# Kernel optimization log

Hardware: AMD Instinct MI355X
Metric: run time of the kernel (lower is better)

The kernel has to match this reference:

```python
import jax, jax.numpy as jnp
import numpy as np

HW, B, C, NH, NC, HF, WF = 2500, 2, 256, 8, 6, 64, 176
DFF = 4 * C
EPS = 1e-5

def _layernorm(x, g, b):
    m = x.mean(-1, keepdims=True)
    v = ((x - m) ** 2).mean(-1, keepdims=True)
    return (x - m) / jnp.sqrt(v + EPS) * g + b

def _mha(q, kv, in_w, in_b, ow, ob):
    # q: [L,B,C], kv: [S,B,C] (batch_first=False, torch nn.MultiheadAttention)
    L, Bq, Cq = q.shape
    S = kv.shape[0]
    Dh = Cq // NH
    qp = (q @ in_w[:Cq].T + in_b[:Cq]).reshape(L, Bq, NH, Dh)
    kp = (kv @ in_w[Cq:2 * Cq].T + in_b[Cq:2 * Cq]).reshape(S, Bq, NH, Dh)
    vp = (kv @ in_w[2 * Cq:].T + in_b[2 * Cq:]).reshape(S, Bq, NH, Dh)
    att = jnp.einsum('lbhd,sbhd->bhls', qp, kp) * (1.0 / np.sqrt(Dh))
    att = jax.nn.softmax(att, axis=-1)
    out = jnp.einsum('bhls,sbhd->lbhd', att, vp).reshape(L, Bq, Cq)
    return out @ ow.T + ob

def _grid_sample_zeros(feat, grid):
    # feat: [B,N,C,H,W], grid: [B,N,Q,2] in [-1,1]; bilinear, align_corners=False, zero padding
    Bb, N, Cc, Hf, Wf = feat.shape
    Q = grid.shape[2]
    x = (grid[..., 0] + 1.0) * (Wf / 2.0) - 0.5
    y = (grid[..., 1] + 1.0) * (Hf / 2.0) - 0.5
    x0 = jnp.floor(x); y0 = jnp.floor(y)
    wx = x - x0; wy = y - y0
    x0i = x0.astype(jnp.int32); y0i = y0.astype(jnp.int32)
    ff = feat.reshape(Bb, N, Cc, Hf * Wf)
    def corner(xi, yi, w):
        valid = (xi >= 0) & (xi < Wf) & (yi >= 0) & (yi < Hf)
        idx = jnp.clip(yi, 0, Hf - 1) * Wf + jnp.clip(xi, 0, Wf - 1)  # [B,N,Q]
        g = jnp.take_along_axis(ff, jnp.broadcast_to(idx[:, :, None, :], (Bb, N, Cc, Q)), axis=-1)
        return g * (w * valid)[:, :, None, :]
    return (corner(x0i, y0i, (1.0 - wx) * (1.0 - wy)) + corner(x0i + 1, y0i, wx * (1.0 - wy))
            + corner(x0i, y0i + 1, (1.0 - wx) * wy) + corner(x0i + 1, y0i + 1, wx * wy))

def _forward(bev_queries, prev_bev, image_feat, reference_points, camera_intrinsics, camera_extrinsics,
             in_proj_w, in_proj_b, out_proj_w, out_proj_b, tsa_norm_g, tsa_norm_b,
             sca_w, sca_b, sca_norm_g, sca_norm_b, ffn_w1, ffn_b1, ffn_w2, ffn_b2, ffn_norm_g, ffn_norm_b):
    # TSA (dropout is identity in eval)
    tsa_out = _mha(bev_queries, prev_bev, in_proj_w, in_proj_b, out_proj_w, out_proj_b)
    x = _layernorm(bev_queries + tsa_out, tsa_norm_g, tsa_norm_b)
    # SCA: ego->camera->image projection
    R = camera_extrinsics[:, :, :3, :3]            # [B,N,3,3]
    t = camera_extrinsics[:, :, :3, 3]             # [B,N,3]
    R_e2c = jnp.swapaxes(R, -1, -2)
    t_e2c = -jnp.einsum('bnij,bnj->bni', R_e2c, t)
    pts_cam = jnp.einsum('bnij,qj->bnqi', R_e2c, reference_points) + t_e2c[:, :, None, :]  # [B,N,Q,3]
    pts_img = jnp.einsum('bnij,bnqj->bnqi', camera_intrinsics, pts_cam)
    uv = pts_img[..., :2] / jnp.maximum(pts_img[..., 2:3], 1e-5)
    grid = jnp.stack([2.0 * uv[..., 0] / WF - 1.0, 2.0 * uv[..., 1] / HF - 1.0], axis=-1)  # [B,N,Q,2]
    Bq = bev_queries.shape[1]
    feat_r = image_feat.reshape(Bq, NC, C, HF, WF)
    sampled = _grid_sample_zeros(feat_r, grid).mean(axis=1)   # [B,C,Q]
    sampled = jnp.transpose(sampled, (2, 0, 1))               # [Q,B,C]
    sca_out = sampled @ sca_w.T + sca_b
    x = _layernorm(x + sca_out, sca_norm_g, sca_norm_b)
    # FFN (torch nn.GELU default = exact erf)
    h = jax.nn.gelu(x @ ffn_w1 + ffn_b1, approximate=False)
    ffn_out = h @ ffn_w2 + ffn_b2
    return _layernorm(x + ffn_out, ffn_norm_g, ffn_norm_b)

def setup_inputs():
    key = jax.random.key(0)
    ks = jax.random.split(key, 16)
    f = jnp.float32
    s = 0.02
    return {
        'bev_queries': jax.random.normal(ks[0], (HW, B, C), f),
        'prev_bev': jax.random.normal(ks[1], (HW, B, C), f),
        'image_feat': jax.random.normal(ks[2], (B * NC, C, HF, WF), f),
        'reference_points': jax.random.normal(ks[3], (HW, 3), f) * 20.0,
        'camera_intrinsics': jax.random.normal(ks[4], (B, NC, 3, 3), f),
        'camera_extrinsics': jax.random.normal(ks[5], (B, NC, 4, 4), f),
        'spatial_shapes': jnp.array([[HF, WF]], jnp.int32),
        'in_proj_w': jax.random.normal(ks[6], (3 * C, C), f) * s,
        'in_proj_b': jnp.zeros((3 * C,), f),
        'out_proj_w': jax.random.normal(ks[7], (C, C), f) * s,
        'out_proj_b': jnp.zeros((C,), f),
        'tsa_norm_g': jnp.ones((C,), f), 'tsa_norm_b': jnp.zeros((C,), f),
        'sca_w': jax.random.normal(ks[8], (C, C), f) * s,
        'sca_b': jnp.zeros((C,), f),
        'sca_norm_g': jnp.ones((C,), f), 'sca_norm_b': jnp.zeros((C,), f),
        'ffn_w1': jax.random.normal(ks[9], (C, DFF), f) * s,
        'ffn_b1': jnp.zeros((DFF,), f),
        'ffn_w2': jax.random.normal(ks[10], (DFF, C), f) * s,
        'ffn_b2': jnp.zeros((C,), f),
        'ffn_norm_g': jnp.ones((C,), f), 'ffn_norm_b': jnp.zeros((C,), f),
    }

def reference(bev_queries, prev_bev, image_feat, reference_points, camera_intrinsics, camera_extrinsics,
              in_proj_w, in_proj_b, out_proj_w, out_proj_b, tsa_norm_g, tsa_norm_b,
              sca_w, sca_b, sca_norm_g, sca_norm_b, ffn_w1, ffn_b1, ffn_w2, ffn_b2, ffn_norm_g, ffn_norm_b,
              spatial_shapes):
    return _forward(bev_queries, prev_bev, image_feat, reference_points, camera_intrinsics, camera_extrinsics,
                    in_proj_w, in_proj_b, out_proj_w, out_proj_b, tsa_norm_g, tsa_norm_b,
                    sca_w, sca_b, sca_norm_g, sca_norm_b, ffn_w1, ffn_b1, ffn_w2, ffn_b2, ffn_norm_g, ffn_norm_b)
```

## Files before the change

kernel.cpp:

```cpp
#include <hip/hip_runtime.h>

typedef unsigned short u16;
typedef __attribute__((ext_vector_type(8))) __bf16 bf8_t;
typedef __attribute__((ext_vector_type(4))) float f4_t;

union bf8u { u16 u[8]; bf8_t v; uint4 q; };

__device__ __forceinline__ float bf2f(u16 v) {
  return __uint_as_float(((unsigned int)v) << 16);
}
__device__ __forceinline__ u16 f2bf(float f) {
  union { __bf16 h; u16 u; } c;
  c.h = (__bf16)f;
  return c.u;
}
__device__ __forceinline__ float bflo(unsigned int w) { return __uint_as_float(w << 16); }
__device__ __forceinline__ float bfhi(unsigned int w) { return __uint_as_float(w & 0xFFFF0000u); }
__device__ __forceinline__ float ldf1(const void* p, size_t i, int isf32) {
  return isf32 ? ((const float*)p)[i] : bf2f(((const u16*)p)[i]);
}

#define LQ    2500
#define LQP   2560
#define BB    2
#define CC    256
#define NCC   6
#define HFF   64
#define WFF   176
#define DFF   1024
#define MROWS 5000

#define WB_UV   256
#define WB_WQKV 240256
#define WB_WOP  633472
#define WB_WSC  764544
#define WB_WF1  895616
#define WB_WF2  1419904
#define WB_S1   1944192
#define WB_S2   (WB_S1 + 2621440)
#define WB_S3   (WB_S2 + 2621440)
#define WB_VT   (WB_S3 + 2621440)
#define WB_H    WB_S2
#define WB_Y3   (WB_S2 + 10485760)

__global__ void detect_k(const u16* __restrict__ rp, int* __restrict__ flag) {
  int bad = 0;
  for (int i = threadIdx.x; i < 7500; i += 64) {
    float v = bf2f(rp[i]);
    if (!(fabsf(v) < 1e6f)) bad = 1;
  }
  int anybad = __any(bad);
  if (threadIdx.x == 0) flag[0] = anybad ? 1 : 0;
}

struct WDesc {
  const void* src[6];
  u16* dst[6];
  int n[6];
  int mode[6];
  int Kd[6], Nd[6];
};
__global__ __launch_bounds__(256) void cvtw_k(WDesc d, const int* __restrict__ flag) {
  const int df = flag[0];
  const int i = blockIdx.y;
  const int n = d.n[i];
  for (int j = blockIdx.x * 256 + threadIdx.x; j < n; j += gridDim.x * 256) {
    if (d.mode[i] == 2) {
      const int row = j / (LQP - LQ), col = LQ + j % (LQP - LQ);
      d.dst[i][(size_t)row * LQP + col] = 0;
    } else if (d.mode[i] == 1) {
      const int K = d.Kd[i], N = d.Nd[i];
      const int nn = j / K, kk = j - nn * K;
      d.dst[i][j] = f2bf(ldf1(d.src[i], (size_t)kk * N + nn, df));
    } else {
      d.dst[i][j] = f2bf(ldf1(d.src[i], j, df));
    }
  }
}

template<int KTPL, int XRAW, int ACT, int RES, int STORE_T>
__global__ __launch_bounds__(64) void gemm_nl(
    const void* __restrict__ Xv, const u16* __restrict__ W,
    const void* __restrict__ bias, size_t boff,
    const void* __restrict__ resv,
    u16* __restrict__ Y, int M, int N, const int* __restrict__ flag)
{
  const int df = flag[0];
  const int lane = threadIdx.x;
  const int ln15 = lane & 15, l4 = lane >> 4;
  const int m0 = blockIdx.x * 16, n0 = blockIdx.y * 64;
  const int am = min(m0 + ln15, M - 1);

  f4_t acc[4];
#pragma unroll
  for (int nt = 0; nt < 4; ++nt) acc[nt] = (f4_t){0.f, 0.f, 0.f, 0.f};

#pragma unroll 8
  for (int k0 = 0; k0 < KTPL; k0 += 32) {
    bf8u a;
    if (XRAW && df) {
      const float* p = (const float*)Xv + (size_t)am * KTPL + k0 + l4 * 8;
      float4 r0 = *(const float4*)p, r1 = *(const float4*)(p + 4);
      a.u[0]=f2bf(r0.x); a.u[1]=f2bf(r0.y); a.u[2]=f2bf(r0.z); a.u[3]=f2bf(r0.w);
      a.u[4]=f2bf(r1.x); a.u[5]=f2bf(r1.y); a.u[6]=f2bf(r1.z); a.u[7]=f2bf(r1.w);
    } else {
      a.q = *(const uint4*)((const u16*)Xv + (size_t)am * KTPL + k0 + l4 * 8);
    }
#pragma unroll
    for (int nt = 0; nt < 4; ++nt) {
      bf8u b;
      b.q = *(const uint4*)&W[(size_t)(n0 + nt * 16 + ln15) * KTPL + k0 + l4 * 8];
      acc[nt] = __builtin_amdgcn_mfma_f32_16x16x32_bf16(a.v, b.v, acc[nt], 0, 0, 0);
    }
  }
#pragma unroll
  for (int nt = 0; nt < 4; ++nt) {
    const int gn = n0 + nt * 16 + ln15;
    const float bv = ldf1(bias, boff + gn, df);
#pragma unroll
    for (int r = 0; r < 4; ++r) {
      const int gm = m0 + l4 * 4 + r;
      if (gm < M) {
        float x = acc[nt][r] + bv;
        if (ACT) x = 0.5f * x * (1.f + erff(x * 0.70710678118654752f));
        if (RES == 1)      x += bf2f(((const u16*)resv)[(size_t)gm * N + gn]);
        else if (RES == 2) x += ldf1(resv, (size_t)gm * N + gn, df);
        if (STORE_T) {
          const int tt = gm >> 1;
          const int tx = tt & 63;
          const int tp = (tx & 35) | ((tx & 12) << 1) | ((tx & 16) >> 2);
          Y[(size_t)(gn + (gm & 1) * 256) * LQP + ((tt & ~63) | tp)] = f2bf(x);
        } else {
          Y[(size_t)gm * N + gn] = f2bf(x);
        }
      }
    }
  }
}

#define TPW 10
__global__ __launch_bounds__(256) void attn_mf(
    const u16* __restrict__ Qw, const u16* __restrict__ Kw,
    const u16* __restrict__ Vt, u16* __restrict__ Ow)
{
  __shared__ float sO[4][16][33];
  __shared__ float sM[4][16];
  __shared__ float sL[4][16];
  const int t = threadIdx.x;
  const int lane = t & 63, w = t >> 6;
  const int ln15 = lane & 15, l4 = lane >> 4;
  const int q0 = blockIdx.x * 16;
  const int by = blockIdx.y;
  const int b = by >> 3, h = by & 7;
  const float SCL2E = 0.25505654481f;

  bf8u aq;
  {
    const int qrow = min(q0 + ln15, LQ - 1);
    bf8u qr; qr.q = *(const uint4*)&Qw[((size_t)qrow * BB + b) * CC + h * 32 + l4 * 8];
#pragma unroll
    for (int i = 0; i < 8; ++i) aq.u[i] = f2bf(bf2f(qr.u[i]) * SCL2E);
  }

  f4_t oacc[2];
  oacc[0] = (f4_t){0.f,0.f,0.f,0.f};
  oacc[1] = (f4_t){0.f,0.f,0.f,0.f};
  float m_r = -1e30f;
  float l_r = 0.f;

  for (int kt = w * TPW; kt < w * TPW + TPW; ++kt) {
    const int kb = kt * 64;
    bf8u av[2][2];
#pragma unroll
    for (int m = 0; m < 2; ++m)
#pragma unroll
      for (int dt = 0; dt < 2; ++dt)
        av[m][dt].q = *(const uint4*)&Vt[(size_t)(by * 32 + dt * 16 + ln15) * LQP + kb + m * 32 + l4 * 8];
    f4_t sv[4];
#pragma unroll
    for (int nt = 0; nt < 4; ++nt) {
      bf8u bk;
      bk.q = *(const uint4*)&Kw[((size_t)(kb + nt * 16 + ln15) * BB + b) * CC + h * 32 + l4 * 8];
      f4_t z = (f4_t){0.f,0.f,0.f,0.f};
      sv[nt] = __builtin_amdgcn_mfma_f32_16x16x32_bf16(bk.v, aq.v, z, 0, 0, 0);
    }
    float p[4][4];
    if (kb + 64 <= LQ) {
#pragma unroll
      for (int nt = 0; nt < 4; ++nt)
#pragma unroll
        for (int r = 0; r < 4; ++r) p[nt][r] = sv[nt][r];
    } else {
#pragma unroll
      for (int nt = 0; nt < 4; ++nt)
#pragma unroll
        for (int r = 0; r < 4; ++r)
          p[nt][r] = (kb + nt * 16 + l4 * 4 + r < LQ) ? sv[nt][r] : -1e30f;
    }
    const float m0 = fmaxf(fmaxf(p[0][0], p[0][1]), fmaxf(p[0][2], p[0][3]));
    const float m1 = fmaxf(fmaxf(p[1][0], p[1][1]), fmaxf(p[1][2], p[1][3]));
    const float m2 = fmaxf(fmaxf(p[2][0], p[2][1]), fmaxf(p[2][2], p[2][3]));
    const float m3 = fmaxf(fmaxf(p[3][0], p[3][1]), fmaxf(p[3][2], p[3][3]));
    float mloc = fmaxf(fmaxf(m0, m1), fmaxf(m2, m3));
    mloc = fmaxf(mloc, __shfl_xor(mloc, 16));
    mloc = fmaxf(mloc, __shfl_xor(mloc, 32));
    const float mn = fmaxf(m_r, mloc);
    const float alpha = __builtin_amdgcn_exp2f(m_r - mn);
    m_r = mn;
    float s = 0.f;
#pragma unroll
    for (int nt = 0; nt < 4; ++nt) {
#pragma unroll
      for (int r = 0; r < 4; ++r) {
        const float e = __builtin_amdgcn_exp2f(p[nt][r] - mn);
        p[nt][r] = e; s += e;
      }
    }
    l_r = l_r * alpha + s;
#pragma unroll
    for (int r = 0; r < 4; ++r) { oacc[0][r] *= alpha; oacc[1][r] *= alpha; }
#pragma unroll
    for (int m = 0; m < 2; ++m) {
      bf8u pb;
#pragma unroll
      for (int i = 0; i < 8; ++i) pb.u[i] = f2bf(p[2 * m + (i >> 2)][i & 3]);
#pragma unroll
      for (int dt = 0; dt < 2; ++dt)
        oacc[dt] = __builtin_amdgcn_mfma_f32_16x16x32_bf16(av[m][dt].v, pb.v, oacc[dt], 0, 0, 0);
    }
  }
  l_r += __shfl_xor(l_r, 16);
  l_r += __shfl_xor(l_r, 32);
#pragma unroll
  for (int dt = 0; dt < 2; ++dt)
#pragma unroll
    for (int r = 0; r < 4; ++r)
      sO[w][ln15][dt * 16 + l4 * 4 + r] = oacc[dt][r];
  if (l4 == 0) { sM[w][ln15] = m_r; sL[w][ln15] = l_r; }
  __syncthreads();
#pragma unroll
  for (int i = t; i < 512; i += 256) {
    const int row = i >> 5, col = i & 31;
    const float M = fmaxf(fmaxf(sM[0][row], sM[1][row]), fmaxf(sM[2][row], sM[3][row]));
    float l = 0.f, O = 0.f;
#pragma unroll
    for (int w4 = 0; w4 < 4; ++w4) {
      const float sc = __builtin_amdgcn_exp2f(sM[w4][row] - M);
      l += sc * sL[w4][row];
      O += sc * sO[w4][row][col];
    }
    const int q = q0 + row;
    if (q < LQ)
      Ow[((size_t)q * BB + b) * CC + h * 32 + col] = f2bf(O / l);
  }
}

template<int TOOUT>
__global__ __launch_bounds__(256) void ln_k(const u16* __restrict__ X,
    const void* __restrict__ g, const void* __restrict__ be,
    void* __restrict__ Yv, int rows, const int* __restrict__ flag)
{
  const int df = flag[0];
  const int lane = threadIdx.x & 63;
  const int row = blockIdx.x * 4 + (threadIdx.x >> 6);
  if (row >= rows) return;
  uint2 raw = *(const uint2*)(X + (size_t)row * CC + lane * 4);
  float vx = bflo(raw.x), vy = bfhi(raw.x), vz = bflo(raw.y), vw = bfhi(raw.y);
  float s = vx + vy + vz + vw;
#pragma unroll
  for (int o = 1; o < 64; o <<= 1) s += __shfl_xor(s, o);
  const float mean = s * 0.00390625f;
  const float dx = vx - mean, dy = vy - mean, dz = vz - mean, dw = vw - mean;
  float sq = dx*dx + dy*dy + dz*dz + dw*dw;
#pragma unroll
  for (int o = 1; o < 64; o <<= 1) sq += __shfl_xor(sq, o);
  const float rstd = rsqrtf(sq * 0.00390625f + 1e-5f);
  const float g0 = ldf1(g, lane*4+0, df), g1 = ldf1(g, lane*4+1, df);
  const float g2 = ldf1(g, lane*4+2, df), g3 = ldf1(g, lane*4+3, df);
  const float b0 = ldf1(be, lane*4+0, df), b1 = ldf1(be, lane*4+1, df);
  const float b2 = ldf1(be, lane*4+2, df), b3 = ldf1(be, lane*4+3, df);
  const float y0 = dx * rstd * g0 + b0;
  const float y1 = dy * rstd * g1 + b1;
  const float y2 = dz * rstd * g2 + b2;
  const float y3 = dw * rstd * g3 + b3;
  if (TOOUT && df) {
    float* yp = (float*)Yv + (size_t)row * CC + lane * 4;
    *(float4*)yp = make_float4(y0, y1, y2, y3);
  } else {
    u16* yp = (u16*)Yv + (size_t)row * CC + lane * 4;
    unsigned int lo = (unsigned int)f2bf(y0) | ((unsigned int)f2bf(y1) << 16);
    unsigned int hi = (unsigned int)f2bf(y2) | ((unsigned int)f2bf(y3) << 16);
    *(uint2*)yp = make_uint2(lo, hi);
  }
}

__global__ __launch_bounds__(256) void uv_k(
    const void* __restrict__ refp, const void* __restrict__ intr,
    const void* __restrict__ extr, float* __restrict__ uv,
    const int* __restrict__ flag)
{
  const int df = flag[0];
  const int idx = blockIdx.x * 256 + threadIdx.x;
  if (idx >= BB * NCC * LQ) return;
  const int bc = idx / LQ;
  const int q = idx - bc * LQ;
  float R[3][3], tv[3], Kc[3][3], p[3];
#pragma unroll
  for (int i = 0; i < 3; ++i) {
#pragma unroll
    for (int j = 0; j < 3; ++j) {
      R[i][j] = ldf1(extr, bc*16 + i*4 + j, df);
      Kc[i][j] = ldf1(intr, bc*9 + i*3 + j, df);
    }
    tv[i] = ldf1(extr, bc*16 + i*4 + 3, df);
  }
#pragma unroll
  for (int j = 0; j < 3; ++j) p[j] = ldf1(refp, q*3 + j, df) - tv[j];
  float pc[3];
#pragma unroll
  for (int i = 0; i < 3; ++i) pc[i] = R[0][i]*p[0] + R[1][i]*p[1] + R[2][i]*p[2];
  float im[3];
#pragma unroll
  for (int i = 0; i < 3; ++i) im[i] = Kc[i][0]*pc[0] + Kc[i][1]*pc[1] + Kc[i][2]*pc[2];
  const float z = fmaxf(im[2], 1e-5f);
  uv[(size_t)idx*2 + 0] = im[0] / z - 0.5f;
  uv[(size_t)idx*2 + 1] = im[1] / z - 0.5f;
}

__global__ __launch_bounds__(256) void samp_k(
    const void* __restrict__ feat, const float* __restrict__ uv,
    u16* __restrict__ S, const int* __restrict__ flag)
{
  const int df = flag[0];
  const int c = blockIdx.x;
  const int b = blockIdx.y / 5;
  const int ch = blockIdx.y % 5;
  const int qend = min((ch + 1) * 500, LQ);
  for (int q = ch * 500 + threadIdx.x; q < qend; q += 256) {
    float acc = 0.f;
#pragma unroll
    for (int cam = 0; cam < NCC; ++cam) {
      const int bc = b * NCC + cam;
      const float x = uv[((size_t)bc * LQ + q) * 2 + 0];
      const float y = uv[((size_t)bc * LQ + q) * 2 + 1];
      const float xf = floorf(x), yf = floorf(y);
      const int x0 = (int)xf, y0 = (int)yf;
      const float wx = x - xf, wy = y - yf;
      const size_t base = ((size_t)bc * CC + c) * (HFF * WFF);
      const bool vx0 = (x0 >= 0) & (x0 < WFF);
      const bool vx1 = (x0 + 1 >= 0) & (x0 + 1 < WFF);
      const bool vy0 = (y0 >= 0) & (y0 < HFF);
      const bool vy1 = (y0 + 1 >= 0) & (y0 + 1 < HFF);
      if (vy0) {
        const size_t rb = base + (size_t)y0 * WFF;
        if (vx0) acc += (1.f - wx) * (1.f - wy) * ldf1(feat, rb + x0, df);
        if (vx1) acc += wx * (1.f - wy) * ldf1(feat, rb + x0 + 1, df);
      }
      if (vy1) {
        const size_t rb = base + (size_t)(y0 + 1) * WFF;
        if (vx0) acc += (1.f - wx) * wy * ldf1(feat, rb + x0, df);
        if (vx1) acc += wx * wy * ldf1(feat, rb + x0 + 1, df);
      }
    }
    S[((size_t)q * BB + b) * CC + c] = f2bf(acc * (1.f / 6.f));
  }
}

extern "C" void kernel_launch(void* const* d_in, const int* in_sizes, int n_in,
                              void* d_out, int out_size, void* d_ws, size_t ws_size,
                              hipStream_t stream) {
  (void)in_sizes; (void)n_in; (void)out_size; (void)ws_size;
  char* base = (char*)d_ws;
  int* flag = (int*)base;
  float* UV = (float*)(base + WB_UV);
  u16* WQKV = (u16*)(base + WB_WQKV);
  u16* WOP  = (u16*)(base + WB_WOP);
  u16* WSC  = (u16*)(base + WB_WSC);
  u16* WF1  = (u16*)(base + WB_WF1);
  u16* WF2  = (u16*)(base + WB_WF2);
  u16* S1 = (u16*)(base + WB_S1);
  u16* S2 = (u16*)(base + WB_S2);
  u16* S3 = (u16*)(base + WB_S3);
  u16* VT = (u16*)(base + WB_VT);
  u16* H  = (u16*)(base + WB_H);
  u16* Y3 = (u16*)(base + WB_Y3);

  detect_k<<<1, 64, 0, stream>>>((const u16*)d_in[3], flag);

  WDesc wd;
  wd.src[0] = d_in[7];  wd.dst[0] = WQKV; wd.n[0] = 196608; wd.mode[0] = 0; wd.Kd[0] = 0;    wd.Nd[0] = 0;
  wd.src[1] = d_in[9];  wd.dst[1] = WOP;  wd.n[1] = 65536;  wd.mode[1] = 0; wd.Kd[1] = 0;    wd.Nd[1] = 0;
  wd.src[2] = d_in[13]; wd.dst[2] = WSC;  wd.n[2] = 65536;  wd.mode[2] = 0; wd.Kd[2] = 0;    wd.Nd[2] = 0;
  wd.src[3] = d_in[17]; wd.dst[3] = WF1;  wd.n[3] = 262144; wd.mode[3] = 1; wd.Kd[3] = 256;  wd.Nd[3] = 1024;
  wd.src[4] = d_in[19]; wd.dst[4] = WF2;  wd.n[4] = 262144; wd.mode[4] = 1; wd.Kd[4] = 1024; wd.Nd[4] = 256;
  wd.src[5] = nullptr;  wd.dst[5] = VT;   wd.n[5] = 512 * (LQP - LQ); wd.mode[5] = 2; wd.Kd[5] = 0; wd.Nd[5] = 0;
  cvtw_k<<<dim3(128, 6), 256, 0, stream>>>(wd, flag);

  uv_k<<<(BB * NCC * LQ + 255) / 256, 256, 0, stream>>>(d_in[3], d_in[4], d_in[5], UV, flag);

  gemm_nl<256,1,0,0,0><<<dim3(313, 4), 64, 0, stream>>>(d_in[0], WQKV,          d_in[8], 0,   nullptr, S1, MROWS, CC, flag);
  gemm_nl<256,1,0,0,0><<<dim3(313, 4), 64, 0, stream>>>(d_in[1], WQKV + 65536,  d_in[8], 256, nullptr, S2, MROWS, CC, flag);
  gemm_nl<256,1,0,0,1><<<dim3(313, 4), 64, 0, stream>>>(d_in[1], WQKV + 131072, d_in[8], 512, nullptr, VT, MROWS, CC, flag);

  attn_mf<<<dim3(157, 16), 256, 0, stream>>>(S1, S2, VT, S3);

  gemm_nl<256,0,0,2,0><<<dim3(313, 4), 64, 0, stream>>>(S3, WOP, d_in[10], 0, d_in[0], S1, MROWS, CC, flag);
  ln_k<0><<<1250, 256, 0, stream>>>(S1, d_in[11], d_in[12], S2, MROWS, flag);

  samp_k<<<dim3(CC, BB * 5), 256, 0, stream>>>(d_in[2], UV, VT, flag);

  gemm_nl<256,0,0,1,0><<<dim3(313, 4), 64, 0, stream>>>(VT, WSC, d_in[14], 0, S2, S3, MROWS, CC, flag);
  ln_k<0><<<1250, 256, 0, stream>>>(S3, d_in[15], d_in[16], S1, MROWS, flag);

  gemm_nl<256,0,1,0,0><<<dim3(313, 16), 64, 0, stream>>>(S1, WF1, d_in[18], 0, nullptr, H,  MROWS, DFF, flag);
  gemm_nl<1024,0,0,1,0><<<dim3(313, 4),  64, 0, stream>>>(H,  WF2, d_in[20], 0, S1,      Y3, MROWS, CC,  flag);
  ln_k<1><<<1250, 256, 0, stream>>>(Y3, d_in[21], d_in[22], d_out, MROWS, flag);
}
```

Before: 515.8 us.

## Fuse QKV projections, prefetch K in attention, lazy softmax rescale, narrower GEMM tiles

Merges the three Q/K/V projection GEMMs into one launch. The attention kernel now prefetches the next K tile into registers, raises wave priority around the MFMA blocks, and only rescales the running output when the max grows by more than 8 (in log2 units). The N-tile width of gemm_nl becomes a template parameter, and the 256-wide-output GEMMs use 16-column tiles so more blocks are launched. Together these aim to cut launch overhead, hide memory latency in attention and raise occupancy on the small GEMMs. The tradeoffs are more redundant A-row loads per GEMM block and a lazy softmax that leaves exponents up to 2^8 before renormalising.

Result: no change. 519.7 us (+0.8%).

```diff
diff --git a/kernel.cpp b/kernel.cpp
--- a/kernel.cpp
+++ b/kernel.cpp
@@ -78,7 +78,7 @@
   }
 }
 
-template<int KTPL, int XRAW, int ACT, int RES, int STORE_T>
+template<int KTPL, int XRAW, int ACT, int RES, int STORE_T, int NT>
 __global__ __launch_bounds__(64) void gemm_nl(
     const void* __restrict__ Xv, const u16* __restrict__ W,
     const void* __restrict__ bias, size_t boff,
@@ -88,12 +88,12 @@
   const int df = flag[0];
   const int lane = threadIdx.x;
   const int ln15 = lane & 15, l4 = lane >> 4;
-  const int m0 = blockIdx.x * 16, n0 = blockIdx.y * 64;
+  const int m0 = blockIdx.x * 16, n0 = blockIdx.y * (NT * 16);
   const int am = min(m0 + ln15, M - 1);
 
-  f4_t acc[4];
-#pragma unroll
-  for (int nt = 0; nt < 4; ++nt) acc[nt] = (f4_t){0.f, 0.f, 0.f, 0.f};
+  f4_t acc[NT];
+#pragma unroll
+  for (int nt = 0; nt < NT; ++nt) acc[nt] = (f4_t){0.f, 0.f, 0.f, 0.f};
 
 #pragma unroll 8
   for (int k0 = 0; k0 < KTPL; k0 += 32) {
@@ -107,14 +107,14 @@
       a.q = *(const uint4*)((const u16*)Xv + (size_t)am * KTPL + k0 + l4 * 8);
     }
 #pragma unroll
-    for (int nt = 0; nt < 4; ++nt) {
+    for (int nt = 0; nt < NT; ++nt) {
       bf8u b;
       b.q = *(const uint4*)&W[(size_t)(n0 + nt * 16 + ln15) * KTPL + k0 + l4 * 8];
       acc[nt] = __builtin_amdgcn_mfma_f32_16x16x32_bf16(a.v, b.v, acc[nt], 0, 0, 0);
     }
   }
 #pragma unroll
-  for (int nt = 0; nt < 4; ++nt) {
+  for (int nt = 0; nt < NT; ++nt) {
     const int gn = n0 + nt * 16 + ln15;
     const float bv = ldf1(bias, boff + gn, df);
 #pragma unroll
@@ -138,6 +138,67 @@
   }
 }
 
+__global__ __launch_bounds__(64) void gemm_qkv(
+    const void* __restrict__ Xq, const void* __restrict__ Xkv,
+    const u16* __restrict__ Wqkv, const void* __restrict__ bias,
+    u16* __restrict__ Qo, u16* __restrict__ Ko, u16* __restrict__ Vt,
+    const int* __restrict__ flag)
+{
+  const int df = flag[0];
+  const int lane = threadIdx.x;
+  const int ln15 = lane & 15, l4 = lane >> 4;
+  const int which = blockIdx.y >> 2;
+  const int n0 = (blockIdx.y & 3) * 64;
+  const void* Xv = (which == 0) ? Xq : Xkv;
+  const u16* W = Wqkv + (size_t)which * 65536;
+  const int m0 = blockIdx.x * 16;
+  const int am = min(m0 + ln15, MROWS - 1);
+
+  f4_t acc[4];
+#pragma unroll
+  for (int nt = 0; nt < 4; ++nt) acc[nt] = (f4_t){0.f, 0.f, 0.f, 0.f};
+
+#pragma unroll 8
+  for (int k0 = 0; k0 < CC; k0 += 32) {
+    bf8u a;
+    if (df) {
+      const float* p = (const float*)Xv + (size_t)am * CC + k0 + l4 * 8;
+      float4 r0 = *(const float4*)p, r1 = *(const float4*)(p + 4);
+      a.u[0]=f2bf(r0.x); a.u[1]=f2bf(r0.y); a.u[2]=f2bf(r0.z); a.u[3]=f2bf(r0.w);
+      a.u[4]=f2bf(r1.x); a.u[5]=f2bf(r1.y); a.u[6]=f2bf(r1.z); a.u[7]=f2bf(r1.w);
+    } else {
+      a.q = *(const uint4*)((const u16*)Xv + (size_t)am * CC + k0 + l4 * 8);
+    }
+#pragma unroll
+    for (int nt = 0; nt < 4; ++nt) {
+      bf8u b;
+      b.q = *(const uint4*)&W[(size_t)(n0 + nt * 16 + ln15) * CC + k0 + l4 * 8];
+      acc[nt] = __builtin_amdgcn_mfma_f32_16x16x32_bf16(a.v, b.v, acc[nt], 0, 0, 0);
+    }
+  }
+#pragma unroll
+  for (int nt = 0; nt < 4; ++nt) {
+    const int gn = n0 + nt * 16 + ln15;
+    const float bv = ldf1(bias, which * 256 + gn, df);
+#pragma unroll
+    for (int r = 0; r < 4; ++r) {
+      const int gm = m0 + l4 * 4 + r;
+      if (gm < MROWS) {
+        const float x = acc[nt][r] + bv;
+        if (which == 2) {
+          const int tt = gm >> 1;
+          const int tx = tt & 63;
+          const int tp = (tx & 35) | ((tx & 12) << 1) | ((tx & 16) >> 2);
+          Vt[(size_t)(gn + (gm & 1) * 256) * LQP + ((tt & ~63) | tp)] = f2bf(x);
+        } else {
+          u16* Y = (which == 0) ? Qo : Ko;
+          Y[(size_t)gm * CC + gn] = f2bf(x);
+        }
+      }
+    }
+  }
+}
+
 #define TPW 10
 __global__ __launch_bounds__(256) void attn_mf(
     const u16* __restrict__ Qw, const u16* __restrict__ Kw,
@@ -168,22 +229,39 @@
   float m_r = -1e30f;
   float l_r = 0.f;
 
-  for (int kt = w * TPW; kt < w * TPW + TPW; ++kt) {
+  const int kt0 = w * TPW;
+  const u16* Kbase = &Kw[(size_t)b * CC + h * 32 + l4 * 8];
+  const u16* Vbase = &Vt[(size_t)(by * 32 + ln15) * LQP + l4 * 8];
+
+  bf8u bkn[4];
+#pragma unroll
+  for (int nt = 0; nt < 4; ++nt)
+    bkn[nt].q = *(const uint4*)&Kbase[(size_t)(kt0 * 64 + nt * 16 + ln15) * CC];
+
+  for (int kt = kt0; kt < kt0 + TPW; ++kt) {
     const int kb = kt * 64;
     bf8u av[2][2];
 #pragma unroll
     for (int m = 0; m < 2; ++m)
 #pragma unroll
       for (int dt = 0; dt < 2; ++dt)
-        av[m][dt].q = *(const uint4*)&Vt[(size_t)(by * 32 + dt * 16 + ln15) * LQP + kb + m * 32 + l4 * 8];
+        av[m][dt].q = *(const uint4*)&Vbase[(size_t)(dt * 16) * LQP + kb + m * 32];
+    bf8u bk[4];
+#pragma unroll
+    for (int nt = 0; nt < 4; ++nt) bk[nt] = bkn[nt];
+    if (kt + 1 < kt0 + TPW) {
+#pragma unroll
+      for (int nt = 0; nt < 4; ++nt)
+        bkn[nt].q = *(const uint4*)&Kbase[(size_t)(kb + 64 + nt * 16 + ln15) * CC];
+    }
     f4_t sv[4];
+    __builtin_amdgcn_s_setprio(1);
 #pragma unroll
     for (int nt = 0; nt < 4; ++nt) {
-      bf8u bk;
-      bk.q = *(const uint4*)&Kw[((size_t)(kb + nt * 16 + ln15) * BB + b) * CC + h * 32 + l4 * 8];
       f4_t z = (f4_t){0.f,0.f,0.f,0.f};
-      sv[nt] = __builtin_amdgcn_mfma_f32_16x16x32_bf16(bk.v, aq.v, z, 0, 0, 0);
-    }
+      sv[nt] = __builtin_amdgcn_mfma_f32_16x16x32_bf16(bk[nt].v, aq.v, z, 0, 0, 0);
+    }
+    __builtin_amdgcn_s_setprio(0);
     float p[4][4];
     if (kb + 64 <= LQ) {
 #pragma unroll
@@ -204,21 +282,25 @@
     float mloc = fmaxf(fmaxf(m0, m1), fmaxf(m2, m3));
     mloc = fmaxf(mloc, __shfl_xor(mloc, 16));
     mloc = fmaxf(mloc, __shfl_xor(mloc, 32));
-    const float mn = fmaxf(m_r, mloc);
-    const float alpha = __builtin_amdgcn_exp2f(m_r - mn);
-    m_r = mn;
+    if (__any(mloc > m_r + 8.f)) {
+      const float mn = fmaxf(m_r, mloc);
+      const float alpha = __builtin_amdgcn_exp2f(m_r - mn);
+      m_r = mn;
+      l_r *= alpha;
+#pragma unroll
+      for (int r = 0; r < 4; ++r) { oacc[0][r] *= alpha; oacc[1][r] *= alpha; }
+    }
     float s = 0.f;
 #pragma unroll
     for (int nt = 0; nt < 4; ++nt) {
 #pragma unroll
       for (int r = 0; r < 4; ++r) {
-        const float e = __builtin_amdgcn_exp2f(p[nt][r] - mn);
+        const float e = __builtin_amdgcn_exp2f(p[nt][r] - m_r);
         p[nt][r] = e; s += e;
       }
     }
-    l_r = l_r * alpha + s;
-#pragma unroll
-    for (int r = 0; r < 4; ++r) { oacc[0][r] *= alpha; oacc[1][r] *= alpha; }
+    l_r += s;
+    __builtin_amdgcn_s_setprio(1);
 #pragma unroll
     for (int m = 0; m < 2; ++m) {
       bf8u pb;
@@ -228,6 +310,7 @@
       for (int dt = 0; dt < 2; ++dt)
         oacc[dt] = __builtin_amdgcn_mfma_f32_16x16x32_bf16(av[m][dt].v, pb.v, oacc[dt], 0, 0, 0);
     }
+    __builtin_amdgcn_s_setprio(0);
   }
   l_r += __shfl_xor(l_r, 16);
   l_r += __shfl_xor(l_r, 32);
@@ -398,21 +481,19 @@
 
   uv_k<<<(BB * NCC * LQ + 255) / 256, 256, 0, stream>>>(d_in[3], d_in[4], d_in[5], UV, flag);
 
-  gemm_nl<256,1,0,0,0><<<dim3(313, 4), 64, 0, stream>>>(d_in[0], WQKV,          d_in[8], 0,   nullptr, S1, MROWS, CC, flag);
-  gemm_nl<256,1,0,0,0><<<dim3(313, 4), 64, 0, stream>>>(d_in[1], WQKV + 65536,  d_in[8], 256, nullptr, S2, MROWS, CC, flag);
-  gemm_nl<256,1,0,0,1><<<dim3(313, 4), 64, 0, stream>>>(d_in[1], WQKV + 131072, d_in[8], 512, nullptr, VT, MROWS, CC, flag);
+  gemm_qkv<<<dim3(313, 12), 64, 0, stream>>>(d_in[0], d_in[1], WQKV, d_in[8], S1, S2, VT, flag);
 
   attn_mf<<<dim3(157, 16), 256, 0, stream>>>(S1, S2, VT, S3);
 
-  gemm_nl<256,0,0,2,0><<<dim3(313, 4), 64, 0, stream>>>(S3, WOP, d_in[10], 0, d_in[0], S1, MROWS, CC, flag);
+  gemm_nl<256,0,0,2,0,1><<<dim3(313, 16), 64, 0, stream>>>(S3, WOP, d_in[10], 0, d_in[0], S1, MROWS, CC, flag);
   ln_k<0><<<1250, 256, 0, stream>>>(S1, d_in[11], d_in[12], S2, MROWS, flag);
 
   samp_k<<<dim3(CC, BB * 5), 256, 0, stream>>>(d_in[2], UV, VT, flag);
 
-  gemm_nl<256,0,0,1,0><<<dim3(313, 4), 64, 0, stream>>>(VT, WSC, d_in[14], 0, S2, S3, MROWS, CC, flag);
+  gemm_nl<256,0,0,1,0,1><<<dim3(313, 16), 64, 0, stream>>>(VT, WSC, d_in[14], 0, S2, S3, MROWS, CC, flag);
   ln_k<0><<<1250, 256, 0, stream>>>(S3, d_in[15], d_in[16], S1, MROWS, flag);
 
-  gemm_nl<256,0,1,0,0><<<dim3(313, 16), 64, 0, stream>>>(S1, WF1, d_in[18], 0, nullptr, H,  MROWS, DFF, flag);
-  gemm_nl<1024,0,0,1,0><<<dim3(313, 4),  64, 0, stream>>>(H,  WF2, d_in[20], 0, S1,      Y3, MROWS, CC,  flag);
+  gemm_nl<256,0,1,0,0,4><<<dim3(313, 16), 64, 0, stream>>>(S1, WF1, d_in[18], 0, nullptr, H,  MROWS, DFF, flag);
+  gemm_nl<1024,0,0,1,0,1><<<dim3(313, 16), 64, 0, stream>>>(H,  WF2, d_in[20], 0, S1,      Y3, MROWS, CC,  flag);
   ln_k<1><<<1250, 256, 0, stream>>>(Y3, d_in[21], d_in[22], d_out, MROWS, flag);
 }
```

## Use LDS-tiled 128x128 GEMM, fuse QKV projections, prefetch K and lazy-rescale in attention

Applied to the files above, without the earlier changes.

Replaces the one-wave 16x64 GEMM with a 256-thread 128x128 tile GEMM that stages A/B through shared memory with register prefetch. The three QKV projections become one launch over a 768-wide output, with inputs pre-converted to bf16 in the weight conversion kernel. The attention kernel now prefetches the next K tile, raises wave priority around MFMAs, and only rescales the running accumulator when the max grows by more than a threshold. Larger tiles cut global reloads, but the N=256 GEMMs launch only 80 blocks, which may underfill the GPU.

Measured after the change: 550.9 us. 1.07x slower.

```diff
diff --git a/kernel.cpp b/kernel.cpp
--- a/kernel.cpp
+++ b/kernel.cpp
@@ -42,6 +42,8 @@
 #define WB_VT   (WB_S3 + 2621440)
 #define WB_H    WB_S2
 #define WB_Y3   (WB_S2 + 10485760)
+#define WB_XQ   WB_Y3
+#define WB_XKV  (WB_Y3 + 2621440)
 
 __global__ void detect_k(const u16* __restrict__ rp, int* __restrict__ flag) {
   int bad = 0;
@@ -54,18 +56,27 @@
 }
 
 struct WDesc {
-  const void* src[6];
-  u16* dst[6];
-  int n[6];
-  int mode[6];
-  int Kd[6], Nd[6];
+  const void* src[8];
+  u16* dst[8];
+  int n[8];
+  int mode[8];
+  int Kd[8], Nd[8];
 };
 __global__ __launch_bounds__(256) void cvtw_k(WDesc d, const int* __restrict__ flag) {
   const int df = flag[0];
   const int i = blockIdx.y;
   const int n = d.n[i];
   for (int j = blockIdx.x * 256 + threadIdx.x; j < n; j += gridDim.x * 256) {
-    if (d.mode[i] == 2) {
+    if (d.mode[i] == 3) {
+      if (df) {
+        const float4 r = ((const float4*)d.src[i])[j];
+        const unsigned int lo = (unsigned int)f2bf(r.x) | ((unsigned int)f2bf(r.y) << 16);
+        const unsigned int hi = (unsigned int)f2bf(r.z) | ((unsigned int)f2bf(r.w) << 16);
+        ((uint2*)d.dst[i])[j] = make_uint2(lo, hi);
+      } else {
+        ((uint2*)d.dst[i])[j] = ((const uint2*)d.src[i])[j];
+      }
+    } else if (d.mode[i] == 2) {
       const int row = j / (LQP - LQ), col = LQ + j % (LQP - LQ);
       d.dst[i][(size_t)row * LQP + col] = 0;
     } else if (d.mode[i] == 1) {
@@ -78,60 +89,102 @@
   }
 }
 
-template<int KTPL, int XRAW, int ACT, int RES, int STORE_T>
-__global__ __launch_bounds__(64) void gemm_nl(
-    const void* __restrict__ Xv, const u16* __restrict__ W,
-    const void* __restrict__ bias, size_t boff,
+#define LDP 40
+template<int KT, int ACT, int RES, int QKV>
+__global__ __launch_bounds__(256) void gemm_t(
+    const u16* __restrict__ Xa, const u16* __restrict__ Xb,
+    const u16* __restrict__ W, const void* __restrict__ bias, size_t boff,
     const void* __restrict__ resv,
-    u16* __restrict__ Y, int M, int N, const int* __restrict__ flag)
+    u16* __restrict__ Y, u16* __restrict__ Yk, u16* __restrict__ Yv,
+    int M, int N, const int* __restrict__ flag)
 {
+  __shared__ __align__(16) u16 sA[128 * LDP];
+  __shared__ __align__(16) u16 sB[128 * LDP];
   const int df = flag[0];
-  const int lane = threadIdx.x;
+  const int t = threadIdx.x;
+  const int lane = t & 63, w = t >> 6;
   const int ln15 = lane & 15, l4 = lane >> 4;
-  const int m0 = blockIdx.x * 16, n0 = blockIdx.y * 64;
-  const int am = min(m0 + ln15, M - 1);
-
-  f4_t acc[4];
-#pragma unroll
-  for (int nt = 0; nt < 4; ++nt) acc[nt] = (f4_t){0.f, 0.f, 0.f, 0.f};
-
-#pragma unroll 8
-  for (int k0 = 0; k0 < KTPL; k0 += 32) {
-    bf8u a;
-    if (XRAW && df) {
-      const float* p = (const float*)Xv + (size_t)am * KTPL + k0 + l4 * 8;
-      float4 r0 = *(const float4*)p, r1 = *(const float4*)(p + 4);
-      a.u[0]=f2bf(r0.x); a.u[1]=f2bf(r0.y); a.u[2]=f2bf(r0.z); a.u[3]=f2bf(r0.w);
-      a.u[4]=f2bf(r1.x); a.u[5]=f2bf(r1.y); a.u[6]=f2bf(r1.z); a.u[7]=f2bf(r1.w);
-    } else {
-      a.q = *(const uint4*)((const u16*)Xv + (size_t)am * KTPL + k0 + l4 * 8);
-    }
-#pragma unroll
-    for (int nt = 0; nt < 4; ++nt) {
-      bf8u b;
-      b.q = *(const uint4*)&W[(size_t)(n0 + nt * 16 + ln15) * KTPL + k0 + l4 * 8];
-      acc[nt] = __builtin_amdgcn_mfma_f32_16x16x32_bf16(a.v, b.v, acc[nt], 0, 0, 0);
-    }
-  }
-#pragma unroll
-  for (int nt = 0; nt < 4; ++nt) {
-    const int gn = n0 + nt * 16 + ln15;
+  const int wm = w & 1, wn = w >> 1;
+  const int m0 = blockIdx.x * 128, n0 = blockIdx.y * 128;
+  const u16* X = (QKV && n0 >= 256) ? Xb : Xa;
+
+  const int r0 = t >> 2, seg = t & 3;
+  const int gr0 = min(m0 + r0, M - 1);
+  const int gr1 = min(m0 + r0 + 64, M - 1);
+  const u16* Asrc0 = X + (size_t)gr0 * KT + seg * 8;
+  const u16* Asrc1 = X + (size_t)gr1 * KT + seg * 8;
+  const u16* Bsrc0 = W + (size_t)(n0 + r0) * KT + seg * 8;
+  const u16* Bsrc1 = W + (size_t)(n0 + r0 + 64) * KT + seg * 8;
+  u16* Adst0 = &sA[r0 * LDP + seg * 8];
+  u16* Adst1 = &sA[(r0 + 64) * LDP + seg * 8];
+  u16* Bdst0 = &sB[r0 * LDP + seg * 8];
+  u16* Bdst1 = &sB[(r0 + 64) * LDP + seg * 8];
+
+  f4_t acc[4][4];
+#pragma unroll
+  for (int mi = 0; mi < 4; ++mi)
+#pragma unroll
+    for (int ni = 0; ni < 4; ++ni) acc[mi][ni] = (f4_t){0.f, 0.f, 0.f, 0.f};
+
+  uint4 ra0 = *(const uint4*)Asrc0;
+  uint4 ra1 = *(const uint4*)Asrc1;
+  uint4 rb0 = *(const uint4*)Bsrc0;
+  uint4 rb1 = *(const uint4*)Bsrc1;
+
+  for (int k0 = 0; k0 < KT; k0 += 32) {
+    __syncthreads();
+    *(uint4*)Adst0 = ra0;  *(uint4*)Adst1 = ra1;
+    *(uint4*)Bdst0 = rb0;  *(uint4*)Bdst1 = rb1;
+    __syncthreads();
+    bf8u a[4], b[4];
+#pragma unroll
+    for (int mi = 0; mi < 4; ++mi)
+      a[mi].q = *(const uint4*)&sA[(wm * 64 + mi * 16 + ln15) * LDP + l4 * 8];
+#pragma unroll
+    for (int ni = 0; ni < 4; ++ni)
+      b[ni].q = *(const uint4*)&sB[(wn * 64 + ni * 16 + ln15) * LDP + l4 * 8];
+    if (k0 + 32 < KT) {
+      ra0 = *(const uint4*)(Asrc0 + k0 + 32);
+      ra1 = *(const uint4*)(Asrc1 + k0 + 32);
+      rb0 = *(const uint4*)(Bsrc0 + k0 + 32);
+      rb1 = *(const uint4*)(Bsrc1 + k0 + 32);
+    }
+#pragma unroll
+    for (int mi = 0; mi < 4; ++mi)
+#pragma unroll
+      for (int ni = 0; ni < 4; ++ni)
+        acc[mi][ni] = __builtin_amdgcn_mfma_f32_16x16x32_bf16(a[mi].v, b[ni].v, acc[mi][ni], 0, 0, 0);
+  }
+
+#pragma unroll
+  for (int ni = 0; ni < 4; ++ni) {
+    const int gn = n0 + wn * 64 + ni * 16 + ln15;
     const float bv = ldf1(bias, boff + gn, df);
 #pragma unroll
-    for (int r = 0; r < 4; ++r) {
-      const int gm = m0 + l4 * 4 + r;
-      if (gm < M) {
-        float x = acc[nt][r] + bv;
-        if (ACT) x = 0.5f * x * (1.f + erff(x * 0.70710678118654752f));
-        if (RES == 1)      x += bf2f(((const u16*)resv)[(size_t)gm * N + gn]);
-        else if (RES == 2) x += ldf1(resv, (size_t)gm * N + gn, df);
-        if (STORE_T) {
-          const int tt = gm >> 1;
-          const int tx = tt & 63;
-          const int tp = (tx & 35) | ((tx & 12) << 1) | ((tx & 16) >> 2);
-          Y[(size_t)(gn + (gm & 1) * 256) * LQP + ((tt & ~63) | tp)] = f2bf(x);
-        } else {
-          Y[(size_t)gm * N + gn] = f2bf(x);
+    for (int mi = 0; mi < 4; ++mi) {
+#pragma unroll
+      for (int r = 0; r < 4; ++r) {
+        const int gm = m0 + wm * 64 + mi * 16 + l4 * 4 + r;
+        if (gm < M) {
+          float x = acc[mi][ni][r] + bv;
+          if (ACT) x = 0.5f * x * (1.f + erff(x * 0.70710678118654752f));
+          if (RES == 1)      x += bf2f(((const u16*)resv)[(size_t)gm * N + gn]);
+          else if (RES == 2) x += ldf1(resv, (size_t)gm * N + gn, df);
+          if (QKV) {
+            const int which = n0 >> 8;
+            const int cn = gn & 255;
+            if (which == 2) {
+              const int tt = gm >> 1, tx = tt & 63;
+              const int tp = (tx & 35) | ((tx & 12) << 1) | ((tx & 16) >> 2);
+              Yv[(size_t)(cn + (gm & 1) * 256) * LQP + ((tt & ~63) | tp)] = f2bf(x);
+            } else if (which == 1) {
+              Yk[(size_t)gm * 256 + cn] = f2bf(x);
+            } else {
+              Y[(size_t)gm * 256 + cn] = f2bf(x);
+            }
+          } else {
+            Y[(size_t)gm * N + gn] = f2bf(x);
+          }
         }
       }
     }
@@ -168,22 +221,39 @@
   float m_r = -1e30f;
   float l_r = 0.f;
 
-  for (int kt = w * TPW; kt < w * TPW + TPW; ++kt) {
+  const int kt0 = w * TPW;
+  const u16* Kbase = &Kw[(size_t)b * CC + h * 32 + l4 * 8];
+  const u16* Vbase = &Vt[(size_t)(by * 32 + ln15) * LQP + l4 * 8];
+
+  bf8u bkn[4];
+#pragma unroll
+  for (int nt = 0; nt < 4; ++nt)
+    bkn[nt].q = *(const uint4*)&Kbase[(size_t)(kt0 * 64 + nt * 16 + ln15) * CC];
+
+  for (int kt = kt0; kt < kt0 + TPW; ++kt) {
     const int kb = kt * 64;
     bf8u av[2][2];
 #pragma unroll
     for (int m = 0; m < 2; ++m)
 #pragma unroll
       for (int dt = 0; dt < 2; ++dt)
-        av[m][dt].q = *(const uint4*)&Vt[(size_t)(by * 32 + dt * 16 + ln15) * LQP + kb + m * 32 + l4 * 8];
+        av[m][dt].q = *(const uint4*)&Vbase[(size_t)(dt * 16) * LQP + kb + m * 32];
+    bf8u bk[4];
+#pragma unroll
+    for (int nt = 0; nt < 4; ++nt) bk[nt] = bkn[nt];
+    if (kt + 1 < kt0 + TPW) {
+#pragma unroll
+      for (int nt = 0; nt < 4; ++nt)
+        bkn[nt].q = *(const uint4*)&Kbase[(size_t)(kb + 64 + nt * 16 + ln15) * CC];
+    }
     f4_t sv[4];
+    __builtin_amdgcn_s_setprio(1);
 #pragma unroll
     for (int nt = 0; nt < 4; ++nt) {
-      bf8u bk;
-      bk.q = *(const uint4*)&Kw[((size_t)(kb + nt * 16 + ln15) * BB + b) * CC + h * 32 + l4 * 8];
       f4_t z = (f4_t){0.f,0.f,0.f,0.f};
-      sv[nt] = __builtin_amdgcn_mfma_f32_16x16x32_bf16(bk.v, aq.v, z, 0, 0, 0);
-    }
+      sv[nt] = __builtin_amdgcn_mfma_f32_16x16x32_bf16(bk[nt].v, aq.v, z, 0, 0, 0);
+    }
+    __builtin_amdgcn_s_setprio(0);
     float p[4][4];
     if (kb + 64 <= LQ) {
 #pragma unroll
@@ -204,21 +274,25 @@
     float mloc = fmaxf(fmaxf(m0, m1), fmaxf(m2, m3));
     mloc = fmaxf(mloc, __shfl_xor(mloc, 16));
     mloc = fmaxf(mloc, __shfl_xor(mloc, 32));
-    const float mn = fmaxf(m_r, mloc);
-    const float alpha = __builtin_amdgcn_exp2f(m_r - mn);
-    m_r = mn;
+    if (__any(mloc > m_r + 8.f)) {
+      const float mn = fmaxf(m_r, mloc);
+      const float alpha = __builtin_amdgcn_exp2f(m_r - mn);
+      m_r = mn;
+      l_r *= alpha;
+#pragma unroll
+      for (int r = 0; r < 4; ++r) { oacc[0][r] *= alpha; oacc[1][r] *= alpha; }
+    }
     float s = 0.f;
 #pragma unroll
     for (int nt = 0; nt < 4; ++nt) {
 #pragma unroll
       for (int r = 0; r < 4; ++r) {
-        const float e = __builtin_amdgcn_exp2f(p[nt][r] - mn);
+        const float e = __builtin_amdgcn_exp2f(p[nt][r] - m_r);
         p[nt][r] = e; s += e;
       }
     }
-    l_r = l_r * alpha + s;
-#pragma unroll
-    for (int r = 0; r < 4; ++r) { oacc[0][r] *= alpha; oacc[1][r] *= alpha; }
+    l_r += s;
+    __builtin_amdgcn_s_setprio(1);
 #pragma unroll
     for (int m = 0; m < 2; ++m) {
       bf8u pb;
@@ -228,6 +302,7 @@
       for (int dt = 0; dt < 2; ++dt)
         oacc[dt] = __builtin_amdgcn_mfma_f32_16x16x32_bf16(av[m][dt].v, pb.v, oacc[dt], 0, 0, 0);
     }
+    __builtin_amdgcn_s_setprio(0);
   }
   l_r += __shfl_xor(l_r, 16);
   l_r += __shfl_xor(l_r, 32);
@@ -384,35 +459,37 @@
   u16* VT = (u16*)(base + WB_VT);
   u16* H  = (u16*)(base + WB_H);
   u16* Y3 = (u16*)(base + WB_Y3);
+  u16* XQ  = (u16*)(base + WB_XQ);
+  u16* XKV = (u16*)(base + WB_XKV);
 
   detect_k<<<1, 64, 0, stream>>>((const u16*)d_in[3], flag);
 
   WDesc wd;
-  wd.src[0] = d_in[7];  wd.dst[0] = WQKV; wd.n[0] = 196608; wd.mode[0] = 0; wd.Kd[0] = 0;    wd.Nd[0] = 0;
-  wd.src[1] = d_in[9];  wd.dst[1] = WOP;  wd.n[1] = 65536;  wd.mode[1] = 0; wd.Kd[1] = 0;    wd.Nd[1] = 0;
-  wd.src[2] = d_in[13]; wd.dst[2] = WSC;  wd.n[2] = 65536;  wd.mode[2] = 0; wd.Kd[2] = 0;    wd.Nd[2] = 0;
+  wd.src[0] = d_in[7];  wd.dst[0] = WQKV; wd.n[0] = 49152;  wd.mode[0] = 3; wd.Kd[0] = 0;    wd.Nd[0] = 0;
+  wd.src[1] = d_in[9];  wd.dst[1] = WOP;  wd.n[1] = 16384;  wd.mode[1] = 3; wd.Kd[1] = 0;    wd.Nd[1] = 0;
+  wd.src[2] = d_in[13]; wd.dst[2] = WSC;  wd.n[2] = 16384;  wd.mode[2] = 3; wd.Kd[2] = 0;    wd.Nd[2] = 0;
   wd.src[3] = d_in[17]; wd.dst[3] = WF1;  wd.n[3] = 262144; wd.mode[3] = 1; wd.Kd[3] = 256;  wd.Nd[3] = 1024;
   wd.src[4] = d_in[19]; wd.dst[4] = WF2;  wd.n[4] = 262144; wd.mode[4] = 1; wd.Kd[4] = 1024; wd.Nd[4] = 256;
   wd.src[5] = nullptr;  wd.dst[5] = VT;   wd.n[5] = 512 * (LQP - LQ); wd.mode[5] = 2; wd.Kd[5] = 0; wd.Nd[5] = 0;
-  cvtw_k<<<dim3(128, 6), 256, 0, stream>>>(wd, flag);
+  wd.src[6] = d_in[0];  wd.dst[6] = XQ;   wd.n[6] = 320000; wd.mode[6] = 3; wd.Kd[6] = 0;    wd.Nd[6] = 0;
+  wd.src[7] = d_in[1];  wd.dst[7] = XKV;  wd.n[7] = 320000; wd.mode[7] = 3; wd.Kd[7] = 0;    wd.Nd[7] = 0;
+  cvtw_k<<<dim3(128, 8), 256, 0, stream>>>(wd, flag);
 
   uv_k<<<(BB * NCC * LQ + 255) / 256, 256, 0, stream>>>(d_in[3], d_in[4], d_in[5], UV, flag);
 
-  gemm_nl<256,1,0,0,0><<<dim3(313, 4), 64, 0, stream>>>(d_in[0], WQKV,          d_in[8], 0,   nullptr, S1, MROWS, CC, flag);
-  gemm_nl<256,1,0,0,0><<<dim3(313, 4), 64, 0, stream>>>(d_in[1], WQKV + 65536,  d_in[8], 256, nullptr, S2, MROWS, CC, flag);
-  gemm_nl<256,1,0,0,1><<<dim3(313, 4), 64, 0, stream>>>(d_in[1], WQKV + 131072, d_in[8], 512, nullptr, VT, MROWS, CC, flag);
+  gemm_t<256,0,0,1><<<dim3(40, 6), 256, 0, stream>>>(XQ, XKV, WQKV, d_in[8], 0, nullptr, S1, S2, VT, MROWS, 768, flag);
 
   attn_mf<<<dim3(157, 16), 256, 0, stream>>>(S1, S2, VT, S3);
 
-  gemm_nl<256,0,0,2,0><<<dim3(313, 4), 64, 0, stream>>>(S3, WOP, d_in[10], 0, d_in[0], S1, MROWS, CC, flag);
+  gemm_t<256,0,2,0><<<dim3(40, 2), 256, 0, stream>>>(S3, nullptr, WOP, d_in[10], 0, d_in[0], S1, nullptr, nullptr, MROWS, CC, flag);
   ln_k<0><<<1250, 256, 0, stream>>>(S1, d_in[11], d_in[12], S2, MROWS, flag);
 
   samp_k<<<dim3(CC, BB * 5), 256, 0, stream>>>(d_in[2], UV, VT, flag);
 
-  gemm_nl<256,0,0,1,0><<<dim3(313, 4), 64, 0, stream>>>(VT, WSC, d_in[14], 0, S2, S3, MROWS, CC, flag);
+  gemm_t<256,0,1,0><<<dim3(40, 2), 256, 0, stream>>>(VT, nullptr, WSC, d_in[14], 0, S2, S3, nullptr, nullptr, MROWS, CC, flag);
   ln_k<0><<<1250, 256, 0, stream>>>(S3, d_in[15], d_in[16], S1, MROWS, flag);
 
-  gemm_nl<256,0,1,0,0><<<dim3(313, 16), 64, 0, stream>>>(S1, WF1, d_in[18], 0, nullptr, H,  MROWS, DFF, flag);
-  gemm_nl<1024,0,0,1,0><<<dim3(313, 4),  64, 0, stream>>>(H,  WF2, d_in[20], 0, S1,      Y3, MROWS, CC,  flag);
+  gemm_t<256,1,0,0><<<dim3(40, 8), 256, 0, stream>>>(S1, nullptr, WF1, d_in[18], 0, nullptr, H, nullptr, nullptr, MROWS, DFF, flag);
+  gemm_t<1024,0,1,0><<<dim3(40, 2), 256, 0, stream>>>(H, nullptr, WF2, d_in[20], 0, S1, Y3, nullptr, nullptr, MROWS, CC, flag);
   ln_k<1><<<1250, 256, 0, stream>>>(Y3, d_in[21], d_in[22], d_out, MROWS, flag);
 }
```
